# Performance work log

Measured on AMD Instinct MI355X. Metric: run time of the kernel, lower is better.

The kernel has to match this reference:

```python
import jax, jax.numpy as jnp
import numpy as np

N = 50000      # nodes
E = 800000     # edges (avg degree 16)
IN_DIM = 128
H = 4          # attention heads
D = 32         # hidden dim per head
NEG_SLOPE = 0.2


def setup_inputs() -> dict:
    key = jax.random.key(0)
    ks = jax.random.split(key, 9)
    x = jax.random.normal(ks[0], (N, IN_DIM), dtype=jnp.float32)
    src = jax.random.randint(ks[1], (E,), 0, N, dtype=jnp.int64)
    dst = jax.random.randint(ks[2], (E,), 0, N, dtype=jnp.int64)
    # layer 0: IN_DIM -> H*D ; layer 1: H*D -> H*D
    s0 = 1.0 / np.sqrt(IN_DIM)
    s1 = 1.0 / np.sqrt(H * D)
    W1 = jax.random.normal(ks[3], (H * D, IN_DIM), dtype=jnp.float32) * s0
    al1 = jax.random.normal(ks[4], (1, H, D), dtype=jnp.float32) * s1
    ar1 = jax.random.normal(ks[5], (1, H, D), dtype=jnp.float32) * s1
    W2 = jax.random.normal(ks[6], (H * D, H * D), dtype=jnp.float32) * s1
    al2 = jax.random.normal(ks[7], (1, H, D), dtype=jnp.float32) * s1
    ar2 = jax.random.normal(ks[8], (1, H, D), dtype=jnp.float32) * s1
    return {"x": x, "src": src, "dst": dst, "W1": W1, "al1": al1, "ar1": ar1,
            "W2": W2, "al2": al2, "ar2": ar2}


def gat_conv(h, src, dst, W, al, ar):
    """DGL-style GATConv. h: [N, F_in] -> [N, H, D], with ELU activation."""
    feat = (h @ W.T).reshape(N, H, D)                 # [N,H,D]
    el = jnp.sum(feat * al, axis=-1)                  # [N,H] a_l . Wh
    er = jnp.sum(feat * ar, axis=-1)                  # [N,H] a_r . Wh
    e = jax.nn.leaky_relu(el[src] + er[dst], NEG_SLOPE)  # [E,H]
    # numerically stable edge softmax over incoming edges of each dst node
    m = jax.ops.segment_max(e, dst, num_segments=N)   # [N,H]
    ee = jnp.exp(e - m[dst])                          # [E,H]
    denom = jax.ops.segment_sum(ee, dst, num_segments=N)  # [N,H]
    alpha = ee / denom[dst]                           # [E,H]
    msg = feat[src] * alpha[..., None]                # [E,H,D]
    out = jax.ops.segment_sum(msg, dst, num_segments=N)   # [N,H,D]
    return jax.nn.elu(out)


def reference(x, src, dst, W1, al1, ar1, W2, al2, ar2):
    h = gat_conv(x, src, dst, W1, al1, ar1).reshape(N, H * D)  # flatten(1)
    h = gat_conv(h, src, dst, W2, al2, ar2)                    # [N,H,D]
    return jnp.mean(h, axis=1)                                 # [N,D]
```

## Files before the change

### kernel.cpp

```cpp
#include <hip/hip_runtime.h>
#include <cmath>
#include <type_traits>

#define HEADS 4
#define FDIM 128
#define NEG 0.2f
#define NBUCK 8
#define EPT 16

typedef __attribute__((ext_vector_type(8))) __bf16 bf16x8;
typedef __attribute__((ext_vector_type(8))) _Float16 h16x8;
typedef __attribute__((ext_vector_type(4))) float f32x4;

__global__ __launch_bounds__(256) void prep_kernel(
    const float* __restrict__ W1, const float* __restrict__ al1,
    const float* __restrict__ ar1,
    const float* __restrict__ W2, const float* __restrict__ al2,
    const float* __restrict__ ar2,
    __bf16* __restrict__ wf1, __bf16* __restrict__ wext1,
    _Float16* __restrict__ wf2, _Float16* __restrict__ wext2,
    int* __restrict__ counts, int nb, int* __restrict__ bsums)
{
    const int b = blockIdx.x, tid = threadIdx.x;
    if (b < 256) {
        int idx = (b & 127) * 256 + tid;
        int j = idx & 7;
        int r = idx >> 3;
        int c = r & 15; r >>= 4;
        int t = r & 7;  r >>= 3;
        int kq = r & 15;
        int hl = r >> 4;
        if (b < 128) {
            float v = W1[(t * 16 + c) * 128 + kq * 8 + j];
            __bf16 hi = (__bf16)v;
            wf1[idx] = (hl == 0) ? hi : (__bf16)(v - (float)hi);
        } else {
            float v = W2[(t * 16 + c) * 128 + kq * 8 + j];
            _Float16 hi = (_Float16)v;
            wf2[idx] = (hl == 0) ? hi : (_Float16)(v - (float)hi);
        }
    } else if (b < 258) {
        const float* W  = (b == 256) ? W1 : W2;
        const float* al = (b == 256) ? al1 : al2;
        const float* ar = (b == 256) ? ar1 : ar2;
        __shared__ float val[1024];
        #pragma unroll
        for (int ch = 0; ch < 4; ++ch) {
            int idx = ch * 256 + tid;
            int c = idx >> 7, k = idx & 127;
            int h = c & 3;
            const float* a = (c < 4) ? al : ar;
            float s = 0.f;
            for (int d = 0; d < 32; ++d)
                s += a[h * 32 + d] * W[(h * 32 + d) * 128 + k];
            val[c * 128 + k] = s;
        }
        __syncthreads();
        #pragma unroll
        for (int ch = 0; ch < 16; ++ch) {
            int idx = tid * 16 + ch;
            int j = idx & 7;
            int r = idx >> 3;
            int c = r & 15; r >>= 4;
            int kq = r & 15;
            int hl = r >> 4;
            float v = (c < 8) ? val[c * 128 + kq * 8 + j] : 0.f;
            if (b == 256) {
                __bf16 hi = (__bf16)v;
                wext1[idx] = (hl == 0) ? hi : (__bf16)(v - (float)hi);
            } else {
                _Float16 hi = (_Float16)v;
                wext2[idx] = (hl == 0) ? hi : (_Float16)(v - (float)hi);
            }
        }
    } else {
        if (b == 258) {
            for (int k = tid; k < 512; k += 256) bsums[k] = 0;
        }
        int i0 = ((b - 258) * 256 + tid) * 4;
        if (i0 + 3 < nb) {
            *(int4*)&counts[i0] = make_int4(0, 0, 0, 0);
        } else {
            for (int i = i0; i < nb; ++i) counts[i] = 0;
        }
    }
}

__device__ __forceinline__ void gemm_body_f32(
    const float* __restrict__ X, const bf16x8* __restrict__ wf,
    const bf16x8* __restrict__ wext, _Float16* __restrict__ featH,
    float* __restrict__ el, float* __restrict__ er,
    int nnodes, int tile0, int tend, int stride, bf16x8* lw)
{
    const int tid = threadIdx.x;
    const int wave = tid >> 6, lane = tid & 63;
    const int l15 = lane & 15, quad = lane >> 4;

    int tile = tile0;
    float xr[32], xn[32];

    auto loadX = [&](int tl, float* dst) {
        int nodeA = tl * 64 + wave * 16 + l15;
        bool v = nodeA < nnodes;
        const float4* xp = (const float4*)(X + (size_t)nodeA * 128);
        #pragma unroll
        for (int ks = 0; ks < 4; ++ks) {
            float4 a = v ? xp[ks * 8 + quad * 2]     : make_float4(0.f, 0.f, 0.f, 0.f);
            float4 b = v ? xp[ks * 8 + quad * 2 + 1] : make_float4(0.f, 0.f, 0.f, 0.f);
            dst[ks * 8 + 0] = a.x; dst[ks * 8 + 1] = a.y;
            dst[ks * 8 + 2] = a.z; dst[ks * 8 + 3] = a.w;
            dst[ks * 8 + 4] = b.x; dst[ks * 8 + 5] = b.y;
            dst[ks * 8 + 6] = b.z; dst[ks * 8 + 7] = b.w;
        }
    };

    loadX(tile, xr);
    for (int i = tid; i < 2048; i += 256) lw[i] = wf[i];
    __syncthreads();

    while (true) {
        int next = tile + stride;
        if (next < tend) loadX(next, xn);

        f32x4 acc[9];
        #pragma unroll
        for (int t = 0; t < 9; ++t) acc[t] = (f32x4){0.f, 0.f, 0.f, 0.f};

        #pragma unroll
        for (int ks = 0; ks < 4; ++ks) {
            bf16x8 ahi, alo;
            #pragma unroll
            for (int j = 0; j < 8; ++j) {
                float xv = xr[ks * 8 + j];
                __bf16 h = (__bf16)xv;
                ahi[j] = h;
                alo[j] = (__bf16)(xv - (float)h);
            }
            const int kq = ks * 4 + quad;

            {
                bf16x8 bh = wext[(kq) * 16 + l15];
                bf16x8 bl = wext[(16 + kq) * 16 + l15];
                acc[8] = __builtin_amdgcn_mfma_f32_16x16x32_bf16(ahi, bh, acc[8], 0, 0, 0);
                acc[8] = __builtin_amdgcn_mfma_f32_16x16x32_bf16(alo, bh, acc[8], 0, 0, 0);
                acc[8] = __builtin_amdgcn_mfma_f32_16x16x32_bf16(ahi, bl, acc[8], 0, 0, 0);
            }
            #pragma unroll
            for (int t = 0; t < 8; ++t) {
                bf16x8 bh = lw[(kq * 8 + t) * 16 + l15];
                bf16x8 bl = wf[2048 + (kq * 8 + t) * 16 + l15];
                acc[t] = __builtin_amdgcn_mfma_f32_16x16x32_bf16(ahi, bh, acc[t], 0, 0, 0);
                acc[t] = __builtin_amdgcn_mfma_f32_16x16x32_bf16(alo, bh, acc[t], 0, 0, 0);
                acc[t] = __builtin_amdgcn_mfma_f32_16x16x32_bf16(ahi, bl, acc[t], 0, 0, 0);
            }
        }

        const int nodeC = tile * 64 + wave * 16 + quad * 4;
        #pragma unroll
        for (int r = 0; r < 4; ++r) {
            int gn = nodeC + r;
            if (gn < nnodes) {
                #pragma unroll
                for (int t = 0; t < 8; ++t)
                    featH[(size_t)gn * 128 + t * 16 + l15] = (_Float16)acc[t][r];
            }
        }
        if (l15 < 8) {
            #pragma unroll
            for (int r = 0; r < 4; ++r) {
                int gn = nodeC + r;
                if (gn < nnodes) {
                    if (l15 < 4) el[gn * HEADS + l15] = acc[8][r];
                    else         er[gn * HEADS + (l15 - 4)] = acc[8][r];
                }
            }
        }

        if (next >= tend) break;
        #pragma unroll
        for (int i = 0; i < 32; ++i) xr[i] = xn[i];
        tile = next;
    }
}

__device__ __forceinline__ void gemm_body_f16(
    const _Float16* __restrict__ X, const h16x8* __restrict__ wf,
    const h16x8* __restrict__ wext, _Float16* __restrict__ featH,
    float* __restrict__ el, float* __restrict__ er,
    int nnodes, int tile0, int tend, int stride, h16x8* lw)
{
    const int tid = threadIdx.x;
    const int wave = tid >> 6, lane = tid & 63;
    const int l15 = lane & 15, quad = lane >> 4;

    int tile = tile0;
    h16x8 xr[4], xn[4];

    auto loadX = [&](int tl, h16x8* dst) {
        int nodeA = tl * 64 + wave * 16 + l15;
        bool v = nodeA < nnodes;
        const h16x8* xp = (const h16x8*)(X + (size_t)nodeA * 128);
        #pragma unroll
        for (int ks = 0; ks < 4; ++ks) {
            if (v) {
                dst[ks] = xp[ks * 4 + quad];
            } else {
                #pragma unroll
                for (int j = 0; j < 8; ++j) dst[ks][j] = (_Float16)0.f;
            }
        }
    };

    loadX(tile, xr);
    for (int i = tid; i < 2048; i += 256) lw[i] = wf[i];
    __syncthreads();

    while (true) {
        int next = tile + stride;
        if (next < tend) loadX(next, xn);

        f32x4 acc[9];
        #pragma unroll
        for (int t = 0; t < 9; ++t) acc[t] = (f32x4){0.f, 0.f, 0.f, 0.f};

        #pragma unroll
        for (int ks = 0; ks < 4; ++ks) {
            h16x8 a = xr[ks];
            const int kq = ks * 4 + quad;
            {
                h16x8 bh = wext[(kq) * 16 + l15];
                h16x8 bl = wext[(16 + kq) * 16 + l15];
                acc[8] = __builtin_amdgcn_mfma_f32_16x16x32_f16(a, bh, acc[8], 0, 0, 0);
                acc[8] = __builtin_amdgcn_mfma_f32_16x16x32_f16(a, bl, acc[8], 0, 0, 0);
            }
            #pragma unroll
            for (int t = 0; t < 8; ++t) {
                h16x8 bh = lw[(kq * 8 + t) * 16 + l15];
                h16x8 bl = wf[2048 + (kq * 8 + t) * 16 + l15];
                acc[t] = __builtin_amdgcn_mfma_f32_16x16x32_f16(a, bh, acc[t], 0, 0, 0);
                acc[t] = __builtin_amdgcn_mfma_f32_16x16x32_f16(a, bl, acc[t], 0, 0, 0);
            }
        }

        const int nodeC = tile * 64 + wave * 16 + quad * 4;
        #pragma unroll
        for (int r = 0; r < 4; ++r) {
            int gn = nodeC + r;
            if (gn < nnodes) {
                #pragma unroll
                for (int t = 0; t < 8; ++t)
                    featH[(size_t)gn * 128 + t * 16 + l15] = (_Float16)acc[t][r];
            }
        }
        if (l15 < 8) {
            #pragma unroll
            for (int r = 0; r < 4; ++r) {
                int gn = nodeC + r;
                if (gn < nnodes) {
                    if (l15 < 4) el[gn * HEADS + l15] = acc[8][r];
                    else         er[gn * HEADS + (l15 - 4)] = acc[8][r];
                }
            }
        }

        if (next >= tend) break;
        #pragma unroll
        for (int i = 0; i < 4; ++i) xr[i] = xn[i];
        tile = next;
    }
}

__device__ __forceinline__ void hist_body(
    const int* __restrict__ src, const int* __restrict__ dst,
    int* __restrict__ counts, int* __restrict__ rank, int nedges, int shift, int b)
{
    int i0 = (b * 256 + threadIdx.x) * EPT;
    if (i0 + EPT - 1 < nedges) {
        int s[EPT], d[EPT], r[EPT];
        #pragma unroll
        for (int q = 0; q < EPT / 4; ++q) {
            *(int4*)&s[q * 4] = *(const int4*)&src[i0 + q * 4];
            *(int4*)&d[q * 4] = *(const int4*)&dst[i0 + q * 4];
        }
        #pragma unroll
        for (int q = 0; q < EPT; ++q)
            r[q] = atomicAdd(&counts[d[q] * NBUCK + (s[q] >> shift)], 1);
        #pragma unroll
        for (int q = 0; q < EPT / 4; ++q)
            *(int4*)&rank[i0 + q * 4] = *(int4*)&r[q * 4];
    } else {
        for (int i = i0; i < nedges; ++i)
            rank[i] = atomicAdd(&counts[dst[i] * NBUCK + (src[i] >> shift)], 1);
    }
}

__device__ __forceinline__ void scatter_body(
    const int* __restrict__ src, const int* __restrict__ dst,
    const int* __restrict__ rank, const int* __restrict__ offsets,
    int* __restrict__ csr_src, int nedges, int shift, int b)
{
    int i0 = (b * 256 + threadIdx.x) * EPT;
    if (i0 + EPT - 1 < nedges) {
        int s[EPT], d[EPT], r[EPT];
        #pragma unroll
        for (int q = 0; q < EPT / 4; ++q) {
            *(int4*)&s[q * 4] = *(const int4*)&src[i0 + q * 4];
            *(int4*)&d[q * 4] = *(const int4*)&dst[i0 + q * 4];
            *(int4*)&r[q * 4] = *(const int4*)&rank[i0 + q * 4];
        }
        int o[EPT];
        #pragma unroll
        for (int q = 0; q < EPT; ++q)
            o[q] = offsets[d[q] * NBUCK + (s[q] >> shift)];
        #pragma unroll
        for (int q = 0; q < EPT; ++q)
            csr_src[o[q] + r[q]] = s[q];
    } else {
        for (int i = i0; i < nedges; ++i)
            csr_src[offsets[dst[i] * NBUCK + (src[i] >> shift)] + rank[i]] = src[i];
    }
}

__global__ __launch_bounds__(256) void fused_gemm_hist(
    const float* __restrict__ X, const bf16x8* __restrict__ wf,
    const bf16x8* __restrict__ wext, _Float16* __restrict__ featH,
    float* __restrict__ el, float* __restrict__ er, int nnodes,
    int t0, int tend, int gemm_blocks, int edge_blocks,
    const int* __restrict__ src, const int* __restrict__ dst,
    int* __restrict__ counts, int* __restrict__ rank, int nedges, int shift)
{
    __shared__ bf16x8 lw[2048];
    if ((int)blockIdx.x >= edge_blocks)
        gemm_body_f32(X, wf, wext, featH, el, er, nnodes,
                      t0 + (blockIdx.x - edge_blocks), tend, gemm_blocks, lw);
    else
        hist_body(src, dst, counts, rank, nedges, shift, blockIdx.x);
}

__global__ __launch_bounds__(256) void fused_gemm_scatter(
    const float* __restrict__ X, const bf16x8* __restrict__ wf,
    const bf16x8* __restrict__ wext, _Float16* __restrict__ featH,
    float* __restrict__ el, float* __restrict__ er, int nnodes,
    int t0, int tend, int gemm_blocks, int edge_blocks,
    const int* __restrict__ src, const int* __restrict__ dst,
    const int* __restrict__ rank, const int* __restrict__ offsets,
    int* __restrict__ csr_src, int nedges, int shift)
{
    __shared__ bf16x8 lw[2048];
    if ((int)blockIdx.x >= edge_blocks)
        gemm_body_f32(X, wf, wext, featH, el, er, nnodes,
                      t0 + (blockIdx.x - edge_blocks), tend, gemm_blocks, lw);
    else
        scatter_body(src, dst, rank, offsets, csr_src, nedges, shift, blockIdx.x);
}

__global__ __launch_bounds__(256) void gemm_mfma_f16_kernel(
    const _Float16* __restrict__ X, const h16x8* __restrict__ wf,
    const h16x8* __restrict__ wext, _Float16* __restrict__ featH,
    float* __restrict__ el, float* __restrict__ er, int nnodes, int ntiles)
{
    __shared__ h16x8 lw[2048];
    gemm_body_f16(X, wf, wext, featH, el, er, nnodes,
                  blockIdx.x, ntiles, gridDim.x, lw);
}

__global__ __launch_bounds__(256) void scan_kernel(
    const int* __restrict__ counts, int* __restrict__ offsets,
    int* __restrict__ pval, int* __restrict__ done, int n, int nedges)
{
    __shared__ int wsums[4];
    const int tid = threadIdx.x, lane = tid & 63, w = tid >> 6;
    const int b = blockIdx.x;
    const int i = b * 1024 + tid * 4;

    int4 v = make_int4(0, 0, 0, 0);
    if (i + 3 < n) v = *(const int4*)&counts[i];
    else {
        if (i < n)     v.x = counts[i];
        if (i + 1 < n) v.y = counts[i + 1];
        if (i + 2 < n) v.z = counts[i + 2];
    }
    int s0 = v.x, s1 = s0 + v.y, s2 = s1 + v.z, s3 = s2 + v.w;

    int x = s3;
    #pragma unroll
    for (int off = 1; off < 64; off <<= 1) {
        int t = __shfl_up(x, off, 64);
        if (lane >= off) x += t;
    }
    if (lane == 63) wsums[w] = x;
    __syncthreads();
    int wbase = 0;
    #pragma unroll
    for (int k = 0; k < 4; ++k) if (k < w) wbase += wsums[k];
    const int total = wsums[0] + wsums[1] + wsums[2] + wsums[3];

    if (tid == 0) {
        pval[b] = total;
        __threadfence();
        atomicAdd(done, 1);
        while (__hip_atomic_load(done, __ATOMIC_ACQUIRE,
                                 __HIP_MEMORY_SCOPE_AGENT) < (int)gridDim.x)
            __builtin_amdgcn_s_sleep(2);
    }
    __syncthreads();

    int basep = 0;
    for (int j = tid; j < b; j += 256) basep += pval[j];
    #pragma unroll
    for (int off = 1; off < 64; off <<= 1) basep += __shfl_xor(basep, off, 64);
    __syncthreads();
    if (lane == 0) wsums[w] = basep;
    __syncthreads();
    const int base = wsums[0] + wsums[1] + wsums[2] + wsums[3];

    const int tbase = base + wbase + x - s3;
    if (i + 3 < n) {
        *(int4*)&offsets[i] = make_int4(tbase, tbase + s0, tbase + s1, tbase + s2);
    } else {
        if (i < n)     offsets[i]     = tbase;
        if (i + 1 < n) offsets[i + 1] = tbase + s0;
        if (i + 2 < n) offsets[i + 2] = tbase + s1;
        if (i + 3 < n) offsets[i + 3] = tbase + s2;
    }
    if (b == 0 && tid == 0) offsets[n] = nedges;
}

template <bool MEAN>
__global__ __launch_bounds__(256) void aggregate_kernel(
    const _Float16* __restrict__ featH, const float* __restrict__ el,
    const float* __restrict__ er, const int* __restrict__ offsets,
    const int* __restrict__ csr_src, void* __restrict__ outp, int nnodes)
{
    const int n = (blockIdx.x * 256 + threadIdx.x) >> 6;
    if (n >= nnodes) return;
    const int lane = threadIdx.x & 63;
    const int g = lane >> 4, u = lane & 15, h = u >> 2;
    const int beg = offsets[n * NBUCK], end = offsets[n * NBUCK + NBUCK];
    const float ern = er[n * HEADS + h];
    const int iters = (end - beg + 3) >> 2;

    float a[8];
    #pragma unroll
    for (int p = 0; p < 8; ++p) a[p] = 0.f;
    float sw = 0.f;

    const h16x8* __restrict__ frow = (const h16x8*)featH;

    int ja = beg + g;
    int jb = ja + 4;
    bool va = ja < end, vb = jb < end;
    int sa = va ? csr_src[ja] : 0;
    int sb = vb ? csr_src[jb] : 0;
    float qa = el[sa * HEADS + h];
    float qb = el[sb * HEADS + h];
    h16x8 fa = frow[(size_t)sa * 16 + u];
    h16x8 fb = frow[(size_t)sb * 16 + u];

    for (int it = 0; it < iters; ++it) {
        int jc = ja + 8;
        bool vc = jc < end;
        int sc = vc ? csr_src[jc] : 0;
        float qc = el[sc * HEADS + h];
        h16x8 fc = frow[(size_t)sc * 16 + u];

        float e = qa + ern;
        e = e > 0.f ? e : NEG * e;
        float w2 = va ? __expf(e) : 0.f;
        #pragma unroll
        for (int p = 0; p < 8; ++p) a[p] += w2 * (float)fa[p];
        sw += w2;

        ja = jb; va = vb; sa = sb; qa = qb; fa = fb;
        jb = jc; vb = vc; sb = sc; qb = qc; fb = fc;
    }

    #pragma unroll
    for (int p = 0; p < 8; ++p) {
        a[p] += __shfl_xor(a[p], 16, 64);
        a[p] += __shfl_xor(a[p], 32, 64);
    }
    sw += __shfl_xor(sw, 16, 64);
    sw += __shfl_xor(sw, 32, 64);

    float inv = sw > 0.f ? 1.f / sw : 0.f;
    float r[8];
    #pragma unroll
    for (int p = 0; p < 8; ++p) {
        float t = a[p] * inv;
        r[p] = t > 0.f ? t : __expf(t) - 1.f;
    }

    if (!MEAN) {
        if (g == 0) {
            h16x8 o;
            #pragma unroll
            for (int p = 0; p < 8; ++p) o[p] = (_Float16)r[p];
            ((h16x8*)outp)[(size_t)n * 16 + u] = o;
        }
    } else {
        #pragma unroll
        for (int p = 0; p < 8; ++p) {
            r[p] += __shfl_xor(r[p], 4, 64);
            r[p] += __shfl_xor(r[p], 8, 64);
        }
        if (g == 0 && u < 4) {
            float* out = (float*)outp;
            float4* o4 = (float4*)(out + (size_t)n * 32 + u * 8);
            o4[0] = make_float4(0.25f * r[0], 0.25f * r[1], 0.25f * r[2], 0.25f * r[3]);
            o4[1] = make_float4(0.25f * r[4], 0.25f * r[5], 0.25f * r[6], 0.25f * r[7]);
        }
    }
}

extern "C" void kernel_launch(void* const* d_in, const int* in_sizes, int n_in,
                              void* d_out, int out_size, void* d_ws, size_t ws_size,
                              hipStream_t stream)
{
    const float* x   = (const float*)d_in[0];
    const int*   src = (const int*)d_in[1];
    const int*   dst = (const int*)d_in[2];
    const float* W1  = (const float*)d_in[3];
    const float* al1 = (const float*)d_in[4];
    const float* ar1 = (const float*)d_in[5];
    const float* W2  = (const float*)d_in[6];
    const float* al2 = (const float*)d_in[7];
    const float* ar2 = (const float*)d_in[8];

    const int N = in_sizes[0] / FDIM;
    const int E = in_sizes[1];
    const int NB = N * NBUCK;

    int shift = 0;
    while (((N - 1) >> shift) > (NBUCK - 1)) ++shift;

    _Float16* h1 = (_Float16*)d_ws;
    _Float16* featH = h1 + (size_t)N * FDIM;
    float* el = (float*)(featH + (size_t)N * FDIM);
    float* er = el + (size_t)N * HEADS;
    int* counts  = (int*)(er + (size_t)N * HEADS);
    int* offsets = counts + NB;
    int* rank    = offsets + (NB + 1);
    int* csr_src = rank + E;
    int* bsums   = csr_src + E;
    uintptr_t wp = ((uintptr_t)(bsums + 512) + 63) & ~(uintptr_t)63;
    __bf16* wf1     = (__bf16*)wp;
    __bf16* wext1   = wf1 + 32768;
    _Float16* wf2   = (_Float16*)(wext1 + 4096);
    _Float16* wext2 = wf2 + 32768;

    const int ntiles = (N + 63) / 64;
    const int halfT  = (ntiles + 1) / 2;
    const int gA = halfT < 256 ? halfT : 256;
    const int gB = (ntiles - halfT) < 256 ? (ntiles - halfT) : 256;
    const int edge_grid = ((E + EPT - 1) / EPT + 255) / 256;
    const int agg_grid  = (N + 3) / 4;
    const int nscan     = (NB + 1023) / 1024;
    const int zblocks   = ((NB + 3) / 4 + 255) / 256;
    const int g2 = ntiles < 512 ? ntiles : 512;

    prep_kernel<<<258 + zblocks, 256, 0, stream>>>(
        W1, al1, ar1, W2, al2, ar2, wf1, wext1, wf2, wext2, counts, NB, bsums);

    fused_gemm_hist<<<edge_grid + gA, 256, 0, stream>>>(
        x, (const bf16x8*)wf1, (const bf16x8*)wext1, featH, el, er, N,
        0, halfT, gA, edge_grid, src, dst, counts, rank, E, shift);

    scan_kernel<<<nscan, 256, 0, stream>>>(counts, offsets, bsums, &bsums[500], NB, E);

    fused_gemm_scatter<<<edge_grid + gB, 256, 0, stream>>>(
        x, (const bf16x8*)wf1, (const bf16x8*)wext1, featH, el, er, N,
        halfT, ntiles, gB, edge_grid, src, dst, rank, offsets, csr_src, E, shift);

    aggregate_kernel<false><<<agg_grid, 256, 0, stream>>>(
        featH, el, er, offsets, csr_src, (void*)h1, N);

    gemm_mfma_f16_kernel<<<g2, 256, 0, stream>>>(
        h1, (const h16x8*)wf2, (const h16x8*)wext2, featH, el, er, N, ntiles);
    aggregate_kernel<true><<<agg_grid, 256, 0, stream>>>(
        featH, el, er, offsets, csr_src, d_out, N);
}
```

Baseline: 262.1 us.

## Replace rank-based CSR scatter with atomic cursors and split scan into two kernels

The histogram pass no longer stores a per-edge rank array. Instead, the scan pass initialises a cursor array from the offsets, and the scatter pass takes each edge's slot with an atomicAdd on that cursor. The single-pass scan, which used a grid-wide spin barrier, is split into a local scan kernel and a base-add kernel. This removes the rank array's write and read traffic and the spin-wait, but adds a second set of atomics in the scatter, one extra kernel launch, and a nondeterministic edge order within each bucket.

Result: no change. 260.2 us (-0.7%).

```diff
diff --git a/kernel.cpp b/kernel.cpp
--- a/kernel.cpp
+++ b/kernel.cpp
@@ -19,7 +19,7 @@
     const float* __restrict__ ar2,
     __bf16* __restrict__ wf1, __bf16* __restrict__ wext1,
     _Float16* __restrict__ wf2, _Float16* __restrict__ wext2,
-    int* __restrict__ counts, int nb, int* __restrict__ bsums)
+    int* __restrict__ counts, int nb)
 {
     const int b = blockIdx.x, tid = threadIdx.x;
     if (b < 256) {
@@ -74,9 +74,6 @@
             }
         }
     } else {
-        if (b == 258) {
-            for (int k = tid; k < 512; k += 256) bsums[k] = 0;
-        }
         int i0 = ((b - 258) * 256 + tid) * 4;
         if (i0 + 3 < nb) {
             *(int4*)&counts[i0] = make_int4(0, 0, 0, 0);
@@ -272,11 +269,11 @@
 
 __device__ __forceinline__ void hist_body(
     const int* __restrict__ src, const int* __restrict__ dst,
-    int* __restrict__ counts, int* __restrict__ rank, int nedges, int shift, int b)
+    int* __restrict__ counts, int nedges, int shift, int b)
 {
     int i0 = (b * 256 + threadIdx.x) * EPT;
     if (i0 + EPT - 1 < nedges) {
-        int s[EPT], d[EPT], r[EPT];
+        int s[EPT], d[EPT];
         #pragma unroll
         for (int q = 0; q < EPT / 4; ++q) {
             *(int4*)&s[q * 4] = *(const int4*)&src[i0 + q * 4];
@@ -284,40 +281,35 @@
         }
         #pragma unroll
         for (int q = 0; q < EPT; ++q)
-            r[q] = atomicAdd(&counts[d[q] * NBUCK + (s[q] >> shift)], 1);
-        #pragma unroll
-        for (int q = 0; q < EPT / 4; ++q)
-            *(int4*)&rank[i0 + q * 4] = *(int4*)&r[q * 4];
+            atomicAdd(&counts[d[q] * NBUCK + (s[q] >> shift)], 1);
     } else {
         for (int i = i0; i < nedges; ++i)
-            rank[i] = atomicAdd(&counts[dst[i] * NBUCK + (src[i] >> shift)], 1);
+            atomicAdd(&counts[dst[i] * NBUCK + (src[i] >> shift)], 1);
     }
 }
 
 __device__ __forceinline__ void scatter_body(
     const int* __restrict__ src, const int* __restrict__ dst,
-    const int* __restrict__ rank, const int* __restrict__ offsets,
-    int* __restrict__ csr_src, int nedges, int shift, int b)
+    int* __restrict__ cursor, int* __restrict__ csr_src,
+    int nedges, int shift, int b)
 {
     int i0 = (b * 256 + threadIdx.x) * EPT;
     if (i0 + EPT - 1 < nedges) {
-        int s[EPT], d[EPT], r[EPT];
+        int s[EPT], d[EPT], p[EPT];
         #pragma unroll
         for (int q = 0; q < EPT / 4; ++q) {
             *(int4*)&s[q * 4] = *(const int4*)&src[i0 + q * 4];
             *(int4*)&d[q * 4] = *(const int4*)&dst[i0 + q * 4];
-            *(int4*)&r[q * 4] = *(const int4*)&rank[i0 + q * 4];
-        }
-        int o[EPT];
+        }
         #pragma unroll
         for (int q = 0; q < EPT; ++q)
-            o[q] = offsets[d[q] * NBUCK + (s[q] >> shift)];
+            p[q] = atomicAdd(&cursor[d[q] * NBUCK + (s[q] >> shift)], 1);
         #pragma unroll
         for (int q = 0; q < EPT; ++q)
-            csr_src[o[q] + r[q]] = s[q];
+            csr_src[p[q]] = s[q];
     } else {
         for (int i = i0; i < nedges; ++i)
-            csr_src[offsets[dst[i] * NBUCK + (src[i] >> shift)] + rank[i]] = src[i];
+            csr_src[atomicAdd(&cursor[dst[i] * NBUCK + (src[i] >> shift)], 1)] = src[i];
     }
 }
 
@@ -327,14 +319,14 @@
     float* __restrict__ el, float* __restrict__ er, int nnodes,
     int t0, int tend, int gemm_blocks, int edge_blocks,
     const int* __restrict__ src, const int* __restrict__ dst,
-    int* __restrict__ counts, int* __restrict__ rank, int nedges, int shift)
+    int* __restrict__ counts, int nedges, int shift)
 {
     __shared__ bf16x8 lw[2048];
     if ((int)blockIdx.x >= edge_blocks)
         gemm_body_f32(X, wf, wext, featH, el, er, nnodes,
                       t0 + (blockIdx.x - edge_blocks), tend, gemm_blocks, lw);
     else
-        hist_body(src, dst, counts, rank, nedges, shift, blockIdx.x);
+        hist_body(src, dst, counts, nedges, shift, blockIdx.x);
 }
 
 __global__ __launch_bounds__(256) void fused_gemm_scatter(
@@ -343,15 +335,14 @@
     float* __restrict__ el, float* __restrict__ er, int nnodes,
     int t0, int tend, int gemm_blocks, int edge_blocks,
     const int* __restrict__ src, const int* __restrict__ dst,
-    const int* __restrict__ rank, const int* __restrict__ offsets,
-    int* __restrict__ csr_src, int nedges, int shift)
+    int* __restrict__ cursor, int* __restrict__ csr_src, int nedges, int shift)
 {
     __shared__ bf16x8 lw[2048];
     if ((int)blockIdx.x >= edge_blocks)
         gemm_body_f32(X, wf, wext, featH, el, er, nnodes,
                       t0 + (blockIdx.x - edge_blocks), tend, gemm_blocks, lw);
     else
-        scatter_body(src, dst, rank, offsets, csr_src, nedges, shift, blockIdx.x);
+        scatter_body(src, dst, cursor, csr_src, nedges, shift, blockIdx.x);
 }
 
 __global__ __launch_bounds__(256) void gemm_mfma_f16_kernel(
@@ -364,14 +355,13 @@
                   blockIdx.x, ntiles, gridDim.x, lw);
 }
 
-__global__ __launch_bounds__(256) void scan_kernel(
+__global__ __launch_bounds__(256) void scan1_kernel(
     const int* __restrict__ counts, int* __restrict__ offsets,
-    int* __restrict__ pval, int* __restrict__ done, int n, int nedges)
+    int* __restrict__ bsums, int n)
 {
     __shared__ int wsums[4];
     const int tid = threadIdx.x, lane = tid & 63, w = tid >> 6;
-    const int b = blockIdx.x;
-    const int i = b * 1024 + tid * 4;
+    const int i = blockIdx.x * 1024 + tid * 4;
 
     int4 v = make_int4(0, 0, 0, 0);
     if (i + 3 < n) v = *(const int4*)&counts[i];
@@ -393,36 +383,38 @@
     int wbase = 0;
     #pragma unroll
     for (int k = 0; k < 4; ++k) if (k < w) wbase += wsums[k];
-    const int total = wsums[0] + wsums[1] + wsums[2] + wsums[3];
-
-    if (tid == 0) {
-        pval[b] = total;
-        __threadfence();
-        atomicAdd(done, 1);
-        while (__hip_atomic_load(done, __ATOMIC_ACQUIRE,
-                                 __HIP_MEMORY_SCOPE_AGENT) < (int)gridDim.x)
-            __builtin_amdgcn_s_sleep(2);
+
+    int tbase = wbase + x - s3;
+    if (i < n)     offsets[i]     = tbase;
+    if (i + 1 < n) offsets[i + 1] = tbase + s0;
+    if (i + 2 < n) offsets[i + 2] = tbase + s1;
+    if (i + 3 < n) offsets[i + 3] = tbase + s2;
+    if (tid == 255) bsums[blockIdx.x] = wbase + x;
+}
+
+__global__ __launch_bounds__(256) void scan23_kernel(
+    int* __restrict__ offsets, int* __restrict__ cursor,
+    const int* __restrict__ bsums, int n, int nedges)
+{
+    __shared__ int sbase;
+    const int tid = threadIdx.x, b = blockIdx.x;
+    if (tid < 64) {
+        int s = 0;
+        for (int i = tid; i < b; i += 64) s += bsums[i];
+        #pragma unroll
+        for (int off = 1; off < 64; off <<= 1) s += __shfl_xor(s, off, 64);
+        if (tid == 0) sbase = s;
     }
     __syncthreads();
-
-    int basep = 0;
-    for (int j = tid; j < b; j += 256) basep += pval[j];
+    const int base = sbase;
+    const int i = b * 1024 + tid * 4;
     #pragma unroll
-    for (int off = 1; off < 64; off <<= 1) basep += __shfl_xor(basep, off, 64);
-    __syncthreads();
-    if (lane == 0) wsums[w] = basep;
-    __syncthreads();
-    const int base = wsums[0] + wsums[1] + wsums[2] + wsums[3];
-
-    const int tbase = base + wbase + x - s3;
-    if (i + 3 < n) {
-        *(int4*)&offsets[i] = make_int4(tbase, tbase + s0, tbase + s1, tbase + s2);
-    } else {
-        if (i < n)     offsets[i]     = tbase;
-        if (i + 1 < n) offsets[i + 1] = tbase + s0;
-        if (i + 2 < n) offsets[i + 2] = tbase + s1;
-        if (i + 3 < n) offsets[i + 3] = tbase + s2;
-    }
+    for (int k = 0; k < 4; ++k)
+        if (i + k < n) {
+            int o = offsets[i + k] + base;
+            offsets[i + k] = o;
+            cursor[i + k] = o;
+        }
     if (b == 0 && tid == 0) offsets[n] = nedges;
 }
 
@@ -540,8 +532,8 @@
     float* er = el + (size_t)N * HEADS;
     int* counts  = (int*)(er + (size_t)N * HEADS);
     int* offsets = counts + NB;
-    int* rank    = offsets + (NB + 1);
-    int* csr_src = rank + E;
+    int* cursor  = offsets + (NB + 1);
+    int* csr_src = cursor + NB;
     int* bsums   = csr_src + E;
     uintptr_t wp = ((uintptr_t)(bsums + 512) + 63) & ~(uintptr_t)63;
     __bf16* wf1     = (__bf16*)wp;
@@ -560,17 +552,18 @@
     const int g2 = ntiles < 512 ? ntiles : 512;
 
     prep_kernel<<<258 + zblocks, 256, 0, stream>>>(
-        W1, al1, ar1, W2, al2, ar2, wf1, wext1, wf2, wext2, counts, NB, bsums);
+        W1, al1, ar1, W2, al2, ar2, wf1, wext1, wf2, wext2, counts, NB);
 
     fused_gemm_hist<<<edge_grid + gA, 256, 0, stream>>>(
         x, (const bf16x8*)wf1, (const bf16x8*)wext1, featH, el, er, N,
-        0, halfT, gA, edge_grid, src, dst, counts, rank, E, shift);
-
-    scan_kernel<<<nscan, 256, 0, stream>>>(counts, offsets, bsums, &bsums[500], NB, E);
+        0, halfT, gA, edge_grid, src, dst, counts, E, shift);
+
+    scan1_kernel<<<nscan, 256, 0, stream>>>(counts, offsets, bsums, NB);
+    scan23_kernel<<<nscan, 256, 0, stream>>>(offsets, cursor, bsums, NB, E);
 
     fused_gemm_scatter<<<edge_grid + gB, 256, 0, stream>>>(
         x, (const bf16x8*)wf1, (const bf16x8*)wext1, featH, el, er, N,
-        halfT, ntiles, gB, edge_grid, src, dst, rank, offsets, csr_src, E, shift);
+        halfT, ntiles, gB, edge_grid, src, dst, cursor, csr_src, E, shift);
 
     aggregate_kernel<false><<<agg_grid, 256, 0, stream>>>(
         featH, el, er, offsets, csr_src, (void*)h1, N);
```
